# Performance work log

Hardware: AMD Instinct MI355X
Metric: run time of the kernel (lower is better)

The kernel has to match this reference:

```python
import jax, jax.numpy as jnp
import numpy as np

N_EDGES = 1_600_000
N_NODES = 100_000
D_FEAT = 64


def setup_inputs() -> dict:
    key = jax.random.key(0)
    k1, k2 = jax.random.split(key)
    messages = jax.random.normal(k1, (N_EDGES, D_FEAT), dtype=jnp.float32)
    dst = jax.random.randint(k2, (N_EDGES,), 0, N_NODES, dtype=jnp.int64)
    return {"messages": messages, "dst": dst, "num_nodes": N_NODES}


def reference(messages, dst, num_nodes):
    # aggregators = ['sum', 'mean', 'max', 'std'] (module default)
    N = num_nodes
    ones = jnp.ones((dst.shape[0],), dtype=messages.dtype)
    # sum aggregation
    s = jax.ops.segment_sum(messages, dst, num_segments=N)  # [N, D]
    # degree, clamped to >= 1 (as in scatter_count)
    deg = jnp.maximum(jax.ops.segment_sum(ones, dst, num_segments=N), 1.0)[:, None]  # [N, 1]
    # mean aggregation
    mean = s / deg
    # max aggregation; empty segments yield -inf -> replaced with 0
    mx = jax.ops.segment_max(messages, dst, num_segments=N)
    mx = jnp.where(jnp.isfinite(mx), mx, jnp.zeros((), dtype=messages.dtype))
    # std aggregation: mean of squared deviations from per-node mean
    sq_diff = (messages - mean[dst]) ** 2
    var = jax.ops.segment_sum(sq_diff, dst, num_segments=N) / deg
    std = jnp.sqrt(var + 1e-8)
    return jnp.concatenate([s, mean, mx, std], axis=-1)  # [N, 4*D]
```

## Files before the change

### kernel.cpp

```cpp
#include <hip/hip_runtime.h>
#include <float.h>


#define BLK 256

typedef float v4f __attribute__((ext_vector_type(4)));

__device__ __forceinline__ v4f fmax4(v4f a, v4f b) {
    v4f r;
    r.x = fmaxf(a.x, b.x); r.y = fmaxf(a.y, b.y);
    r.z = fmaxf(a.z, b.z); r.w = fmaxf(a.w, b.w);
    return r;
}

__global__ void zero_counts(int* __restrict__ counts, int N) {
    int i = blockIdx.x * BLK + threadIdx.x;
    if (i < N) counts[i] = 0;
}

__global__ void hist_rank(const int* __restrict__ dst, int stride,
                          int* __restrict__ counts, int* __restrict__ rank, int E) {
    int p = blockIdx.x * BLK + threadIdx.x;
    int npair = E >> 1;
    if (p < npair) {
        int n0, n1;
        if (stride == 2) { int4 v = ((const int4*)dst)[p]; n0 = v.x; n1 = v.z; }
        else             { int2 v = ((const int2*)dst)[p]; n0 = v.x; n1 = v.y; }
        int r0 = atomicAdd(&counts[n0], 1);
        int r1 = atomicAdd(&counts[n1], 1);
        *(int2*)(rank + 2 * p) = make_int2(r0, r1);
    }
    if ((E & 1) && p == npair) {
        int e = E - 1;
        int n = (stride == 2) ? (int)((const long long*)dst)[e] : dst[e];
        rank[e] = atomicAdd(&counts[n], 1);
    }
}

__global__ void scatter_rank(const int* __restrict__ dst, int stride,
                             const int* __restrict__ lofs, const int* __restrict__ partials,
                             const int* __restrict__ rank, int* __restrict__ perm, int E) {
    int p = blockIdx.x * BLK + threadIdx.x;
    int npair = E >> 1;
    if (p < npair) {
        int n0, n1;
        if (stride == 2) { int4 v = ((const int4*)dst)[p]; n0 = v.x; n1 = v.z; }
        else             { int2 v = ((const int2*)dst)[p]; n0 = v.x; n1 = v.y; }
        int2 r = *(const int2*)(rank + 2 * p);
        perm[lofs[n0] + partials[n0 >> 8] + r.x] = 2 * p;
        perm[lofs[n1] + partials[n1 >> 8] + r.y] = 2 * p + 1;
    }
    if ((E & 1) && p == npair) {
        int e = E - 1;
        int n = (stride == 2) ? (int)((const long long*)dst)[e] : dst[e];
        perm[lofs[n] + partials[n >> 8] + rank[e]] = e;
    }
}

__global__ void scan1(const int* __restrict__ counts, int* __restrict__ lofs,
                      int* __restrict__ partials, int N) {
    __shared__ int s[BLK];
    int t = threadIdx.x;
    int i = blockIdx.x * BLK + t;
    int x = (i < N) ? counts[i] : 0;
    s[t] = x;
    __syncthreads();
    for (int o = 1; o < BLK; o <<= 1) {
        int y = (t >= o) ? s[t - o] : 0;
        __syncthreads();
        s[t] += y;
        __syncthreads();
    }
    if (i < N) lofs[i] = s[t] - x;
    if (t == BLK - 1) partials[blockIdx.x] = s[t];
}

__global__ void scan2(int* __restrict__ partials, int NB) {
    __shared__ int s[512];
    int t = threadIdx.x;
    int x = (t < NB) ? partials[t] : 0;
    s[t] = x;
    __syncthreads();
    for (int o = 1; o < 512; o <<= 1) {
        int y = (t >= o) ? s[t - o] : 0;
        __syncthreads();
        s[t] += y;
        __syncthreads();
    }
    if (t < NB) partials[t] = s[t] - x;
}

__global__ void hist(const int* __restrict__ dst, int stride, int* __restrict__ counts, int E) {
    int e = blockIdx.x * BLK + threadIdx.x;
    if (e < E) {
        int n = (stride == 2) ? (int)((const long long*)dst)[e] : dst[e];
        atomicAdd(&counts[n], 1);
    }
}

__global__ void cursor_init(const int* __restrict__ lofs, const int* __restrict__ partials,
                            int* __restrict__ cursor, int N) {
    int i = blockIdx.x * BLK + threadIdx.x;
    if (i < N) cursor[i] = lofs[i] + partials[i >> 8];
}

__global__ void permscatter(const int* __restrict__ dst, int stride,
                            int* __restrict__ cursor, int* __restrict__ perm, int E) {
    int e = blockIdx.x * BLK + threadIdx.x;
    if (e < E) {
        int n = (stride == 2) ? (int)((const long long*)dst)[e] : dst[e];
        int pos = atomicAdd(&cursor[n], 1);
        perm[pos] = e;
    }
}

__global__ void reduce(const float* __restrict__ msg, const int* __restrict__ perm,
                       const int* __restrict__ lofs, const int* __restrict__ partials,
                       const int* __restrict__ counts, float* __restrict__ out, int N) {
    int node = blockIdx.x * 4 + (threadIdx.x >> 6);
    if (node >= N) return;
    int lane = threadIdx.x & 63;
    int qid  = lane >> 4;
    int fq   = lane & 15;

    int beg   = lofs[node] + partials[node >> 8];
    int deg_i = counts[node];
    int end   = beg + deg_i;

    v4f s4 = {0.f, 0.f, 0.f, 0.f};
    v4f q4 = {0.f, 0.f, 0.f, 0.f};
    v4f m4 = {-FLT_MAX, -FLT_MAX, -FLT_MAX, -FLT_MAX};

    const v4f* __restrict__ msg4 = (const v4f*)msg;

    for (int base = beg; base < end; base += 64) {
        int cnt = end - base;
        if (cnt > 64) cnt = 64;
        int idx = base + lane;
        if (idx >= end) idx = end - 1;
        int eid_l = perm[idx];

        int j = 0;
        for (; j + 8 <= cnt; j += 8) {
            int ea = __shfl(eid_l, j + qid);
            int eb = __shfl(eid_l, j + 4 + qid);
            v4f va = __builtin_nontemporal_load(msg4 + (((long long)ea << 4) + fq));
            v4f vb = __builtin_nontemporal_load(msg4 + (((long long)eb << 4) + fq));
            s4 += va; q4 += va * va; m4 = fmax4(m4, va);
            s4 += vb; q4 += vb * vb; m4 = fmax4(m4, vb);
        }
        int rem = cnt - j;
        if (rem > 0) {
            int sa = j + qid;
            int ea = __shfl(eid_l, (sa < cnt) ? sa : (cnt - 1));
            v4f va = __builtin_nontemporal_load(msg4 + (((long long)ea << 4) + fq));
            if (sa < cnt) { s4 += va; q4 += va * va; m4 = fmax4(m4, va); }
            if (rem > 4) {
                int sb = j + 4 + qid;
                int eb = __shfl(eid_l, (sb < cnt) ? sb : (cnt - 1));
                v4f vb = __builtin_nontemporal_load(msg4 + (((long long)eb << 4) + fq));
                if (sb < cnt) { s4 += vb; q4 += vb * vb; m4 = fmax4(m4, vb); }
            }
        }
    }

    #pragma unroll
    for (int off = 16; off <= 32; off <<= 1) {
        s4.x += __shfl_xor(s4.x, off); s4.y += __shfl_xor(s4.y, off);
        s4.z += __shfl_xor(s4.z, off); s4.w += __shfl_xor(s4.w, off);
        q4.x += __shfl_xor(q4.x, off); q4.y += __shfl_xor(q4.y, off);
        q4.z += __shfl_xor(q4.z, off); q4.w += __shfl_xor(q4.w, off);
        m4.x = fmaxf(m4.x, __shfl_xor(m4.x, off));
        m4.y = fmaxf(m4.y, __shfl_xor(m4.y, off));
        m4.z = fmaxf(m4.z, __shfl_xor(m4.z, off));
        m4.w = fmaxf(m4.w, __shfl_xor(m4.w, off));
    }

    if (qid == 0) {
        float deg = fmaxf((float)deg_i, 1.0f);
        v4f mean = s4 / deg;
        v4f var  = q4 / deg - mean * mean;
        var.x = fmaxf(var.x, 0.f); var.y = fmaxf(var.y, 0.f);
        var.z = fmaxf(var.z, 0.f); var.w = fmaxf(var.w, 0.f);
        v4f stdv;
        stdv.x = sqrtf(var.x + 1e-8f); stdv.y = sqrtf(var.y + 1e-8f);
        stdv.z = sqrtf(var.z + 1e-8f); stdv.w = sqrtf(var.w + 1e-8f);
        v4f mx = m4;
        if (deg_i == 0) { mx.x = 0.f; mx.y = 0.f; mx.z = 0.f; mx.w = 0.f; }

        v4f* bo = (v4f*)(out + (long long)node * 256);
        __builtin_nontemporal_store(s4,   bo + fq);
        __builtin_nontemporal_store(mean, bo + 16 + fq);
        __builtin_nontemporal_store(mx,   bo + 32 + fq);
        __builtin_nontemporal_store(stdv, bo + 48 + fq);
    }
}

extern "C" void kernel_launch(void* const* d_in, const int* in_sizes, int n_in,
                              void* d_out, int out_size, void* d_ws, size_t ws_size,
                              hipStream_t stream) {
    const float* msg = (const float*)d_in[0];
    const int*   dst = (const int*)d_in[1];
    float* out = (float*)d_out;

    int E = in_sizes[0] / 64;
    int N = out_size / 256;
    int stride = (in_sizes[1] == 2 * E) ? 2 : 1;

    int* counts   = (int*)d_ws;
    int* lofs     = counts + N;
    int* partials = lofs + N;
    int* perm     = partials + 512;
    int* extra    = perm + E;

    int NB_N = (N + BLK - 1) / BLK;
    int NB_E = (E + BLK - 1) / BLK;
    int NT_P = ((E + 1) >> 1);
    int NB_P = (NT_P + BLK - 1) / BLK;

    size_t need_rank = ((size_t)2 * N + 512 + (size_t)2 * E) * sizeof(int);

    zero_counts<<<NB_N, BLK, 0, stream>>>(counts, N);

    if (ws_size >= need_rank) {
        int* rank = extra;
        hist_rank<<<NB_P, BLK, 0, stream>>>(dst, stride, counts, rank, E);
        scan1<<<NB_N, BLK, 0, stream>>>(counts, lofs, partials, N);
        scan2<<<1, 512, 0, stream>>>(partials, NB_N);
        scatter_rank<<<NB_P, BLK, 0, stream>>>(dst, stride, lofs, partials, rank, perm, E);
    } else {
        int* cursor = extra;
        hist<<<NB_E, BLK, 0, stream>>>(dst, stride, counts, E);
        scan1<<<NB_N, BLK, 0, stream>>>(counts, lofs, partials, N);
        scan2<<<1, 512, 0, stream>>>(partials, NB_N);
        cursor_init<<<NB_N, BLK, 0, stream>>>(lofs, partials, cursor, N);
        permscatter<<<NB_E, BLK, 0, stream>>>(dst, stride, cursor, perm, E);
    }

    reduce<<<(N + 3) / 4, BLK, 0, stream>>>(msg, perm, lofs, partials, counts, out, N);
}
```

Measured before the change: 642.2 us.

## Widen hist/scatter to four edges per thread and enlarge reduce blocks

The histogram-rank and scatter-rank kernels now handle four edges per thread with 128-bit loads of dst and rank, and write rank with nontemporal stores. Zeroing of counts is vectorized. The reduce kernel now runs 512-thread blocks holding eight nodes each, and loads perm with nontemporal loads. The aim is fewer memory instructions and less launch overhead in the preprocessing stages. The risk is lower occupancy or poorer latency hiding for the atomics, since each thread now issues more of them.

```diff
diff --git a/kernel.cpp b/kernel.cpp
--- a/kernel.cpp
+++ b/kernel.cpp
@@ -3,8 +3,10 @@
 
 
 #define BLK 256
+#define RBLK 512
 
 typedef float v4f __attribute__((ext_vector_type(4)));
+typedef int   v4i __attribute__((ext_vector_type(4)));
 
 __device__ __forceinline__ v4f fmax4(v4f a, v4f b) {
     v4f r;
@@ -15,23 +17,34 @@
 
 __global__ void zero_counts(int* __restrict__ counts, int N) {
     int i = blockIdx.x * BLK + threadIdx.x;
-    if (i < N) counts[i] = 0;
+    int n4 = N >> 2;
+    if (i < n4) ((v4i*)counts)[i] = (v4i){0, 0, 0, 0};
+    if (i < (N & 3)) counts[(n4 << 2) + i] = 0;
 }
 
 __global__ void hist_rank(const int* __restrict__ dst, int stride,
                           int* __restrict__ counts, int* __restrict__ rank, int E) {
-    int p = blockIdx.x * BLK + threadIdx.x;
-    int npair = E >> 1;
-    if (p < npair) {
-        int n0, n1;
-        if (stride == 2) { int4 v = ((const int4*)dst)[p]; n0 = v.x; n1 = v.z; }
-        else             { int2 v = ((const int2*)dst)[p]; n0 = v.x; n1 = v.y; }
+    int g = blockIdx.x * BLK + threadIdx.x;
+    int ng = E >> 2;
+    if (g < ng) {
+        int n0, n1, n2, n3;
+        if (stride == 2) {
+            v4i a = ((const v4i*)dst)[2 * g];
+            v4i b = ((const v4i*)dst)[2 * g + 1];
+            n0 = a.x; n1 = a.z; n2 = b.x; n3 = b.z;
+        } else {
+            v4i a = ((const v4i*)dst)[g];
+            n0 = a.x; n1 = a.y; n2 = a.z; n3 = a.w;
+        }
         int r0 = atomicAdd(&counts[n0], 1);
         int r1 = atomicAdd(&counts[n1], 1);
-        *(int2*)(rank + 2 * p) = make_int2(r0, r1);
-    }
-    if ((E & 1) && p == npair) {
-        int e = E - 1;
+        int r2 = atomicAdd(&counts[n2], 1);
+        int r3 = atomicAdd(&counts[n3], 1);
+        v4i rv = {r0, r1, r2, r3};
+        __builtin_nontemporal_store(rv, (v4i*)rank + g);
+    }
+    if (g < (E & 3)) {
+        int e = (ng << 2) + g;
         int n = (stride == 2) ? (int)((const long long*)dst)[e] : dst[e];
         rank[e] = atomicAdd(&counts[n], 1);
     }
@@ -40,18 +53,27 @@
 __global__ void scatter_rank(const int* __restrict__ dst, int stride,
                              const int* __restrict__ lofs, const int* __restrict__ partials,
                              const int* __restrict__ rank, int* __restrict__ perm, int E) {
-    int p = blockIdx.x * BLK + threadIdx.x;
-    int npair = E >> 1;
-    if (p < npair) {
-        int n0, n1;
-        if (stride == 2) { int4 v = ((const int4*)dst)[p]; n0 = v.x; n1 = v.z; }
-        else             { int2 v = ((const int2*)dst)[p]; n0 = v.x; n1 = v.y; }
-        int2 r = *(const int2*)(rank + 2 * p);
-        perm[lofs[n0] + partials[n0 >> 8] + r.x] = 2 * p;
-        perm[lofs[n1] + partials[n1 >> 8] + r.y] = 2 * p + 1;
-    }
-    if ((E & 1) && p == npair) {
-        int e = E - 1;
+    int g = blockIdx.x * BLK + threadIdx.x;
+    int ng = E >> 2;
+    if (g < ng) {
+        int n0, n1, n2, n3;
+        if (stride == 2) {
+            v4i a = ((const v4i*)dst)[2 * g];
+            v4i b = ((const v4i*)dst)[2 * g + 1];
+            n0 = a.x; n1 = a.z; n2 = b.x; n3 = b.z;
+        } else {
+            v4i a = ((const v4i*)dst)[g];
+            n0 = a.x; n1 = a.y; n2 = a.z; n3 = a.w;
+        }
+        v4i r = __builtin_nontemporal_load((const v4i*)rank + g);
+        int e = 4 * g;
+        perm[lofs[n0] + partials[n0 >> 8] + r.x] = e;
+        perm[lofs[n1] + partials[n1 >> 8] + r.y] = e + 1;
+        perm[lofs[n2] + partials[n2 >> 8] + r.z] = e + 2;
+        perm[lofs[n3] + partials[n3 >> 8] + r.w] = e + 3;
+    }
+    if (g < (E & 3)) {
+        int e = (ng << 2) + g;
         int n = (stride == 2) ? (int)((const long long*)dst)[e] : dst[e];
         perm[lofs[n] + partials[n >> 8] + rank[e]] = e;
     }
@@ -114,10 +136,11 @@
     }
 }
 
-__global__ void reduce(const float* __restrict__ msg, const int* __restrict__ perm,
-                       const int* __restrict__ lofs, const int* __restrict__ partials,
-                       const int* __restrict__ counts, float* __restrict__ out, int N) {
-    int node = blockIdx.x * 4 + (threadIdx.x >> 6);
+__global__ void __launch_bounds__(RBLK) reduce(
+        const float* __restrict__ msg, const int* __restrict__ perm,
+        const int* __restrict__ lofs, const int* __restrict__ partials,
+        const int* __restrict__ counts, float* __restrict__ out, int N) {
+    int node = blockIdx.x * 8 + (threadIdx.x >> 6);
     if (node >= N) return;
     int lane = threadIdx.x & 63;
     int qid  = lane >> 4;
@@ -138,7 +161,7 @@
         if (cnt > 64) cnt = 64;
         int idx = base + lane;
         if (idx >= end) idx = end - 1;
-        int eid_l = perm[idx];
+        int eid_l = __builtin_nontemporal_load(perm + idx);
 
         int j = 0;
         for (; j + 8 <= cnt; j += 8) {
@@ -215,19 +238,19 @@
 
     int NB_N = (N + BLK - 1) / BLK;
     int NB_E = (E + BLK - 1) / BLK;
-    int NT_P = ((E + 1) >> 1);
-    int NB_P = (NT_P + BLK - 1) / BLK;
+    int NB_Z = ((N >> 2) + BLK - 1) / BLK;
+    int NB_G = ((E >> 2) + BLK - 1) / BLK;
 
     size_t need_rank = ((size_t)2 * N + 512 + (size_t)2 * E) * sizeof(int);
 
-    zero_counts<<<NB_N, BLK, 0, stream>>>(counts, N);
+    zero_counts<<<NB_Z, BLK, 0, stream>>>(counts, N);
 
     if (ws_size >= need_rank) {
         int* rank = extra;
-        hist_rank<<<NB_P, BLK, 0, stream>>>(dst, stride, counts, rank, E);
+        hist_rank<<<NB_G, BLK, 0, stream>>>(dst, stride, counts, rank, E);
         scan1<<<NB_N, BLK, 0, stream>>>(counts, lofs, partials, N);
         scan2<<<1, 512, 0, stream>>>(partials, NB_N);
-        scatter_rank<<<NB_P, BLK, 0, stream>>>(dst, stride, lofs, partials, rank, perm, E);
+        scatter_rank<<<NB_G, BLK, 0, stream>>>(dst, stride, lofs, partials, rank, perm, E);
     } else {
         int* cursor = extra;
         hist<<<NB_E, BLK, 0, stream>>>(dst, stride, counts, E);
@@ -237,5 +260,5 @@
         permscatter<<<NB_E, BLK, 0, stream>>>(dst, stride, cursor, perm, E);
     }
 
-    reduce<<<(N + 3) / 4, BLK, 0, stream>>>(msg, perm, lofs, partials, counts, out, N);
-}
+    reduce<<<(N + 7) / 8, RBLK, 0, stream>>>(msg, perm, lofs, partials, counts, out, N);
+}
```

Measured after the change: 658.6 us. +2.6%, slower.
